# Kernel tuning notes

Hardware: AMD Instinct MI355X
Metric: run time of the kernel (lower is better)

Reference implementation:

```python
import jax, jax.numpy as jnp
import numpy as np

B, S, H = 4, 512, 1024
E, K, I = 8, 2, 2048

def setup_inputs() -> dict:
    key = jax.random.key(0)
    k1, k2, k3, k4, k5 = jax.random.split(key, 5)
    scale_h = 1.0 / np.sqrt(H)
    scale_i = 1.0 / np.sqrt(I)
    return {
        "hidden_states": jax.random.normal(k1, (B, S, H), dtype=jnp.float32),
        "router_w": jax.random.normal(k2, (E, H), dtype=jnp.float32) * scale_h,
        "w_gate": jax.random.normal(k3, (E, H, I), dtype=jnp.float32) * scale_h,
        "w_up": jax.random.normal(k4, (E, H, I), dtype=jnp.float32) * scale_h,
        "w_down": jax.random.normal(k5, (E, I, H), dtype=jnp.float32) * scale_i,
    }

def reference(hidden_states, router_w, w_gate, w_up, w_down):
    b, s, h = hidden_states.shape
    x = hidden_states.reshape(-1, h)              # [T, H] tokens
    T = x.shape[0]

    # ---- RouterTopK: fp32 linear -> softmax over all experts -> top-k ----
    router_logits = x.astype(jnp.float32) @ router_w.T          # [T, E]
    probs = jax.nn.softmax(router_logits, axis=-1)               # [T, E]
    top_vals, top_idx = jax.lax.top_k(probs, K)                  # [T, K]

    # normalize_top_k_affinities (norm_topk_prob=True)
    top_vals = top_vals / jnp.sum(top_vals, axis=-1, keepdims=True)

    # scatter normalized affinities into a dense [T, E] combine matrix
    aff = jnp.zeros((T, E), dtype=x.dtype).at[jnp.arange(T)[:, None], top_idx].set(top_vals.astype(x.dtype))

    # ---- ExpertMLPs: GLU (swiglu) per expert, combine weighted by affinity ----
    # Dense-per-expert computation; non-selected experts contribute 0 via aff.
    gate = jnp.einsum('th,ehi->eti', x, w_gate)                  # [E, T, I]
    up = jnp.einsum('th,ehi->eti', x, w_up)                      # [E, T, I]
    act = jax.nn.silu(gate) * up                                 # [E, T, I]
    expert_out = jnp.einsum('eti,eih->eth', act, w_down)         # [E, T, H]
    out = jnp.einsum('eth,te->th', expert_out, aff)              # [T, H]

    # _reduce_output: all-reduce over TP/world group -> identity single-device
    return out.reshape(b, s, h)
```

## Files before the change

### kernel.cpp

```cpp
#include <hip/hip_runtime.h>
#include <hip/hip_bf16.h>

#define T_TOK 2048
#define H_DIM 1024
#define E_N   8
#define I_DIM 2048
#define GW    4096

#define NT_MAX 24
#define SLOTS  6144

typedef unsigned short u16;
typedef unsigned int   u32;
typedef __bf16 bf16_t;
typedef bf16_t bf16x8 __attribute__((ext_vector_type(8)));
typedef u16    u16x8  __attribute__((ext_vector_type(8)));
typedef u16    u16x4  __attribute__((ext_vector_type(4)));
typedef float  f32x16 __attribute__((ext_vector_type(16)));

#define MFMA32 __builtin_amdgcn_mfma_f32_32x32x16_bf16
#define SB()   __builtin_amdgcn_sched_barrier(0)

__device__ __forceinline__ u16 bfbits(float f) {
    bf16_t b = (bf16_t)f;
    return __builtin_bit_cast(u16, b);
}
__device__ __forceinline__ float bf2f(u16 u) {
    u32 x = ((u32)u) << 16;
    return __builtin_bit_cast(float, x);
}

__device__ __forceinline__ void gload_lds16(const void* g, void* l) {
    __builtin_amdgcn_global_load_lds(
        (const __attribute__((address_space(1))) void*)g,
        (__attribute__((address_space(3))) void*)l, 16, 0, 0);
}

__device__ __forceinline__ int tile_off(int n, int kb) {
    return n * 64 + ((kb ^ ((n >> 1) & 7)) << 3);
}
__device__ __forceinline__ int a_off(int row, int kslot) {
    return row * 64 + ((kslot ^ (row & 7)) << 3);
}

__global__ __launch_bounds__(256) void router_k(
    const float* __restrict__ x, const float* __restrict__ rw,
    int* __restrict__ cnt, int* __restrict__ tok,
    int4* __restrict__ invA, float2* __restrict__ invW,
    u16* __restrict__ xbf)
{
    int wid = threadIdx.x >> 6, lane = threadIdx.x & 63;
    int t = blockIdx.x * 4 + wid;
    const float* xr = x + (size_t)t * H_DIM;
    u16* xbr = xbf + (size_t)t * H_DIM;

    float acc[E_N];
#pragma unroll
    for (int e = 0; e < E_N; e++) acc[e] = 0.f;
#pragma unroll
    for (int j = 0; j < H_DIM / 256; j++) {
        int o = lane * 4 + j * 256;
        float4 xv = *reinterpret_cast<const float4*>(xr + o);
        u16x4 p;
        p[0] = bfbits(xv.x); p[1] = bfbits(xv.y); p[2] = bfbits(xv.z); p[3] = bfbits(xv.w);
        *reinterpret_cast<u16x4*>(xbr + o) = p;
#pragma unroll
        for (int e = 0; e < E_N; e++) {
            float4 wv = *reinterpret_cast<const float4*>(rw + e * H_DIM + o);
            acc[e] += xv.x * wv.x + xv.y * wv.y + xv.z * wv.z + xv.w * wv.w;
        }
    }
#pragma unroll
    for (int e = 0; e < E_N; e++) {
        float v = acc[e];
        for (int off = 32; off; off >>= 1) v += __shfl_xor(v, off);
        acc[e] = v;
    }
    if (lane == 0) {
        int i0 = 0; float m0 = acc[0];
#pragma unroll
        for (int e = 1; e < E_N; e++) if (acc[e] > m0) { m0 = acc[e]; i0 = e; }
        int i1 = -1; float m1 = -INFINITY;
#pragma unroll
        for (int e = 0; e < E_N; e++) if (e != i0 && acc[e] > m1) { m1 = acc[e]; i1 = e; }
        float w0 = 1.f / (1.f + expf(m1 - m0));
        float w1 = 1.f - w0;
        int p0 = atomicAdd(&cnt[i0], 1);
        tok[i0 * T_TOK + p0] = t;
        int p1 = atomicAdd(&cnt[i1], 1);
        tok[i1 * T_TOK + p1] = t;
        invA[t] = make_int4(i0, p0, i1, p1);
        invW[t] = make_float2(w0, w1);
    }
}

__global__ void prefix_k(const int* __restrict__ cnt, int* __restrict__ offs_pad,
                         int* __restrict__ tile_e, int* __restrict__ tile_row0,
                         int* __restrict__ ntiles)
{
    if (threadIdx.x == 0) {
        int s = 0, nt = 0;
        for (int e = 0; e < E_N; e++) {
            offs_pad[e] = s;
            int c = cnt[e];
            int t = (c + 255) >> 8;
            for (int i = 0; i < t; i++) { tile_e[nt] = e; tile_row0[nt] = i * 256; nt++; }
            s += t * 256;
        }
        offs_pad[E_N] = s;
        *ntiles = nt;
    }
}

__global__ __launch_bounds__(512, 4) void gu_k(
    const u16* __restrict__ xbf, const float* __restrict__ wg, const float* __restrict__ wu,
    const int* __restrict__ cnt, const int* __restrict__ offs_pad,
    const int* __restrict__ tile_e, const int* __restrict__ tile_row0,
    const int* __restrict__ ntiles, const int* __restrict__ tok,
    u16* __restrict__ gbuf)
{
    int q = gridDim.x >> 3;
    int phys = blockIdx.x;
    int logical = (phys & 7) * q + (phys >> 3);
    int tb = logical % NT_MAX;
    int p  = logical / NT_MAX;
    if (tb >= *ntiles) return;
    int e = tile_e[tb], row0 = tile_row0[tb];
    int cntE = cnt[e];
    int slot0 = offs_pad[e] + row0;
    int n0 = p * 128;
    int mat  = n0 >> 11;
    int coln = n0 & 2047;

    __shared__ u16 AS[2][16384], BS[8192];

    int tid = threadIdx.x;
    int lane = tid & 63, wid = tid >> 6;
    int wm = wid >> 1, wn = wid & 1;
    int l31 = lane & 31, lh = lane >> 5;

    const u16* asrc[4];
#pragma unroll
    for (int i = 0; i < 4; i++) {
        int row = wid * 32 + i * 8 + (lane >> 3);
        int rc = (row0 + row < cntE) ? (row0 + row) : (cntE - 1);
        asrc[i] = xbf + (size_t)tok[e * T_TOK + rc] * H_DIM
                  + (((lane & 7) ^ ((lane >> 3) & 7)) << 3);
    }
    int s0 = wid * 2048;

    int bn = tid & 127;
    int kq = tid >> 7;
    const float* wsrc = (mat ? wu : wg) + (size_t)e * H_DIM * I_DIM + coln + bn;

    float v[16];

#define BLOAD(t) { \
    _Pragma("unroll") \
    for (int j = 0; j < 16; j++) \
        v[j] = wsrc[(size_t)((t) * 64 + kq * 16 + j) * I_DIM]; }

#define BWRITE() { \
    _Pragma("unroll") \
    for (int jb = 0; jb < 2; jb++) { \
        u16x8 pk; \
        _Pragma("unroll") \
        for (int jj = 0; jj < 8; jj++) pk[jj] = bfbits(v[jb * 8 + jj]); \
        *reinterpret_cast<u16x8*>(&BS[tile_off(bn, kq * 2 + jb)]) = pk; } }

#define ASTAGE(nbuf, t) { \
    _Pragma("unroll") \
    for (int i = 0; i < 4; i++) \
        gload_lds16(asrc[i] + (size_t)(t) * 64, &AS[nbuf][s0 + i * 512]); }

    f32x16 acc[2][2];
#pragma unroll
    for (int a = 0; a < 2; a++)
#pragma unroll
        for (int b = 0; b < 2; b++) acc[a][b] = (f32x16)0.f;

#define CLUSTER(bufi) { \
    _Pragma("unroll") \
    for (int ks = 0; ks < 4; ks++) { \
        bf16x8 af[2], bfr[2]; \
        _Pragma("unroll") \
        for (int mf = 0; mf < 2; mf++) \
            af[mf] = *reinterpret_cast<const bf16x8*>(&AS[bufi][a_off(wm * 64 + mf * 32 + l31, ks * 2 + lh)]); \
        _Pragma("unroll") \
        for (int nf = 0; nf < 2; nf++) \
            bfr[nf] = *reinterpret_cast<const bf16x8*>(&BS[tile_off(wn * 64 + nf * 32 + l31, ks * 2 + lh)]); \
        _Pragma("unroll") \
        for (int mf = 0; mf < 2; mf++) \
            _Pragma("unroll") \
            for (int nf = 0; nf < 2; nf++) \
                acc[mf][nf] = MFMA32(af[mf], bfr[nf], acc[mf][nf], 0, 0, 0); } }

    ASTAGE(0, 0);
    SB();
    BLOAD(0);
    SB();
    BWRITE();
    SB();
    asm volatile("s_waitcnt vmcnt(0) lgkmcnt(0)" ::: "memory");
    __builtin_amdgcn_s_barrier();
    SB();

    for (int t = 0; t < 16; t++) {
        int ab = t & 1;
        bool more = (t + 1) < 16;
        if (more) {
            ASTAGE(ab ^ 1, t + 1);
            SB();
            BLOAD(t + 1);
            SB();
        }
        CLUSTER(ab);
        SB();
        __builtin_amdgcn_s_barrier();
        SB();
        if (more) {
            BWRITE();
            SB();
            asm volatile("s_waitcnt vmcnt(0) lgkmcnt(0)" ::: "memory");
            __builtin_amdgcn_s_barrier();
            SB();
        }
    }
#undef BLOAD
#undef BWRITE
#undef ASTAGE
#undef CLUSTER

#pragma unroll
    for (int mf = 0; mf < 2; mf++)
#pragma unroll
        for (int nf = 0; nf < 2; nf++) {
            int col = n0 + wn * 64 + nf * 32 + l31;
#pragma unroll
            for (int r = 0; r < 16; r++) {
                int rl = wm * 64 + mf * 32 + (r & 3) + 8 * (r >> 2) + 4 * lh;
                gbuf[(size_t)(slot0 + rl) * GW + col] = bfbits(acc[mf][nf][r]);
            }
        }
}

__global__ __launch_bounds__(256) void act_k(u16* __restrict__ gbuf)
{
    int s = blockIdx.x;
    int i = threadIdx.x * 8;
    u16x8 g8 = *reinterpret_cast<const u16x8*>(&gbuf[(size_t)s * GW + i]);
    u16x8 u8 = *reinterpret_cast<const u16x8*>(&gbuf[(size_t)s * GW + 2048 + i]);
    u16x8 o;
#pragma unroll
    for (int j = 0; j < 8; j++) {
        float g = bf2f(g8[j]);
        float u = bf2f(u8[j]);
        o[j] = bfbits(g / (1.f + expf(-g)) * u);
    }
    *reinterpret_cast<u16x8*>(&gbuf[(size_t)s * GW + i]) = o;
}

__global__ __launch_bounds__(512, 4) void down_k(
    const u16* __restrict__ gbuf, const float* __restrict__ wd,
    const int* __restrict__ cnt, const int* __restrict__ offs_pad,
    const int* __restrict__ tile_e, const int* __restrict__ tile_row0,
    const int* __restrict__ ntiles, const int* __restrict__ tok,
    u16* __restrict__ dbuf)
{
    int q = gridDim.x >> 3;
    int phys = blockIdx.x;
    int logical = (phys & 7) * q + (phys >> 3);
    int tb = logical % NT_MAX;
    int rest = logical / NT_MAX;
    int p   = rest & 7;
    int kq4 = rest >> 3;
    if (tb >= *ntiles) return;
    int e = tile_e[tb], row0 = tile_row0[tb];
    int slot0 = offs_pad[e] + row0;
    int h0 = p * 128;

    __shared__ u16 AS[2][16384], BS[8192];

    int tid = threadIdx.x;
    int lane = tid & 63, wid = tid >> 6;
    int wm = wid >> 1, wn = wid & 1;
    int l31 = lane & 31, lh = lane >> 5;

    const u16* asrc[4];
#pragma unroll
    for (int i = 0; i < 4; i++) {
        int row = wid * 32 + i * 8 + (lane >> 3);
        asrc[i] = gbuf + (size_t)(slot0 + row) * GW + kq4 * 512
                  + (((lane & 7) ^ ((lane >> 3) & 7)) << 3);
    }
    int s0 = wid * 2048;

    int bn = tid & 127;
    int kq = tid >> 7;
    const float* dsrc = wd + ((size_t)e * I_DIM + kq4 * 512) * H_DIM + h0 + bn;

    float v[16];

#define BLOAD(t) { \
    _Pragma("unroll") \
    for (int j = 0; j < 16; j++) \
        v[j] = dsrc[(size_t)((t) * 64 + kq * 16 + j) * H_DIM]; }

#define BWRITE() { \
    _Pragma("unroll") \
    for (int jb = 0; jb < 2; jb++) { \
        u16x8 pk; \
        _Pragma("unroll") \
        for (int jj = 0; jj < 8; jj++) pk[jj] = bfbits(v[jb * 8 + jj]); \
        *reinterpret_cast<u16x8*>(&BS[tile_off(bn, kq * 2 + jb)]) = pk; } }

#define ASTAGE(nbuf, t) { \
    _Pragma("unroll") \
    for (int i = 0; i < 4; i++) \
        gload_lds16(asrc[i] + (size_t)(t) * 64, &AS[nbuf][s0 + i * 512]); }

    f32x16 acc[2][2];
#pragma unroll
    for (int a = 0; a < 2; a++)
#pragma unroll
        for (int b = 0; b < 2; b++) acc[a][b] = (f32x16)0.f;

#define CLUSTER(bufi) { \
    _Pragma("unroll") \
    for (int ks = 0; ks < 4; ks++) { \
        bf16x8 af[2], bfr[2]; \
        _Pragma("unroll") \
        for (int mf = 0; mf < 2; mf++) \
            af[mf] = *reinterpret_cast<const bf16x8*>(&AS[bufi][a_off(wm * 64 + mf * 32 + l31, ks * 2 + lh)]); \
        _Pragma("unroll") \
        for (int nf = 0; nf < 2; nf++) \
            bfr[nf] = *reinterpret_cast<const bf16x8*>(&BS[tile_off(wn * 64 + nf * 32 + l31, ks * 2 + lh)]); \
        _Pragma("unroll") \
        for (int mf = 0; mf < 2; mf++) \
            _Pragma("unroll") \
            for (int nf = 0; nf < 2; nf++) \
                acc[mf][nf] = MFMA32(af[mf], bfr[nf], acc[mf][nf], 0, 0, 0); } }

    ASTAGE(0, 0);
    SB();
    BLOAD(0);
    SB();
    BWRITE();
    SB();
    asm volatile("s_waitcnt vmcnt(0) lgkmcnt(0)" ::: "memory");
    __builtin_amdgcn_s_barrier();
    SB();

    for (int t = 0; t < 8; t++) {
        int ab = t & 1;
        bool more = (t + 1) < 8;
        if (more) {
            ASTAGE(ab ^ 1, t + 1);
            SB();
            BLOAD(t + 1);
            SB();
        }
        CLUSTER(ab);
        SB();
        __builtin_amdgcn_s_barrier();
        SB();
        if (more) {
            BWRITE();
            SB();
            asm volatile("s_waitcnt vmcnt(0) lgkmcnt(0)" ::: "memory");
            __builtin_amdgcn_s_barrier();
            SB();
        }
    }
#undef BLOAD
#undef BWRITE
#undef ASTAGE
#undef CLUSTER

#pragma unroll
    for (int mf = 0; mf < 2; mf++)
#pragma unroll
        for (int nf = 0; nf < 2; nf++) {
            int col = h0 + wn * 64 + nf * 32 + l31;
#pragma unroll
            for (int r = 0; r < 16; r++) {
                int rl = wm * 64 + mf * 32 + (r & 3) + 8 * (r >> 2) + 4 * lh;
                dbuf[(size_t)(kq4 * SLOTS + slot0 + rl) * H_DIM + col] = bfbits(acc[mf][nf][r]);
            }
        }
}

__global__ __launch_bounds__(256) void gather_k(
    const u16* __restrict__ dbuf, const int4* __restrict__ invA,
    const float2* __restrict__ invW, const int* __restrict__ offs_pad,
    float* __restrict__ out)
{
    int t = blockIdx.x;
    int h = threadIdx.x * 4;
    int4 ia = invA[t];
    float2 w = invW[t];
    int s0 = offs_pad[ia.x] + ia.y;
    int s1 = offs_pad[ia.z] + ia.w;

    float4 o = make_float4(0.f, 0.f, 0.f, 0.f);
    float* op = &o.x;
#pragma unroll
    for (int qk = 0; qk < 4; qk++) {
        u16x4 a = *reinterpret_cast<const u16x4*>(&dbuf[(size_t)(qk * SLOTS + s0) * H_DIM + h]);
        u16x4 b = *reinterpret_cast<const u16x4*>(&dbuf[(size_t)(qk * SLOTS + s1) * H_DIM + h]);
#pragma unroll
        for (int j = 0; j < 4; j++)
            op[j] += w.x * bf2f(a[j]) + w.y * bf2f(b[j]);
    }
    *reinterpret_cast<float4*>(&out[(size_t)t * H_DIM + h]) = o;
}

extern "C" void kernel_launch(void* const* d_in, const int* in_sizes, int n_in,
                              void* d_out, int out_size, void* d_ws, size_t ws_size,
                              hipStream_t stream)
{
    const float* x  = (const float*)d_in[0];
    const float* rw = (const float*)d_in[1];
    const float* wg = (const float*)d_in[2];
    const float* wu = (const float*)d_in[3];
    const float* wd = (const float*)d_in[4];
    float* out = (float*)d_out;

    char* ws = (char*)d_ws;
    int*    cnt       = (int*)(ws);
    int*    ntiles    = (int*)(ws + 32);
    int*    offs_pad  = (int*)(ws + 64);
    int*    tile_e    = (int*)(ws + 256);
    int*    tile_row0 = (int*)(ws + 512);
    int*    tok       = (int*)(ws + 64 * 1024);
    int4*   invA      = (int4*)(ws + 160 * 1024);
    float2* invW      = (float2*)(ws + 200 * 1024);
    u16*    xbf       = (u16*)(ws + 256 * 1024);
    u16*    gbuf      = (u16*)(ws + 5ull * 1024 * 1024);
    u16*    dbuf      = (u16*)(ws + 53ull * 1024 * 1024);

    size_t need = 102ull * 1024 * 1024;
    if (ws_size < need) return;

    hipMemsetAsync(cnt, 0, 32, stream);

    router_k<<<T_TOK / 4, 256, 0, stream>>>(x, rw, cnt, tok, invA, invW, xbf);
    prefix_k<<<1, 64, 0, stream>>>(cnt, offs_pad, tile_e, tile_row0, ntiles);
    gu_k<<<NT_MAX * (GW / 128), 512, 0, stream>>>(
        xbf, wg, wu, cnt, offs_pad, tile_e, tile_row0, ntiles, tok, gbuf);
    act_k<<<SLOTS, 256, 0, stream>>>(gbuf);
    down_k<<<NT_MAX * (H_DIM / 128) * 4, 512, 0, stream>>>(
        gbuf, wd, cnt, offs_pad, tile_e, tile_row0, ntiles, tok, dbuf);
    gather_k<<<T_TOK, 256, 0, stream>>>(dbuf, invA, invW, offs_pad, out);
}
```

Measured before the change: 211.6 us.

## Restructure expert GEMM main loops into fine-grained software pipeline, halve down split-K

Replaces the per-tile load/compute/store loop in both expert GEMM kernels with an interleaved STEP schedule. Each MFMA sub-step overlaps async A staging, a partial B conversion write into a double-buffered B LDS tile, and register prefetch of B two tiles ahead. MFMAs run under raised priority and waits use a partial vmcnt. The down projection split-K goes from 4 to 2 chunks of 1024, which halves the partial-output buffer and gather reads but doubles per-block work and halves the grid. Launch bounds drop to 2 blocks per SM to fit the extra registers and LDS.

```diff
diff --git a/kernel.cpp b/kernel.cpp
--- a/kernel.cpp
+++ b/kernel.cpp
@@ -112,7 +112,62 @@
     }
 }
 
-__global__ __launch_bounds__(512, 4) void gu_k(
+#define STEP(tt, WSET, LSET, BUFI)                                              \
+  {                                                                             \
+    bool m1 = (tt) + 1 < 16, m2 = (tt) + 2 < 16;                                \
+    _Pragma("unroll")                                                           \
+    for (int p = 0; p < 4; p++) {                                               \
+      bf16x8 af0 = *reinterpret_cast<const bf16x8*>(                            \
+          &AS[BUFI][a_off(wm * 64 + l31, p * 2 + lh)]);                         \
+      bf16x8 af1 = *reinterpret_cast<const bf16x8*>(                            \
+          &AS[BUFI][a_off(wm * 64 + 32 + l31, p * 2 + lh)]);                    \
+      bf16x8 bf0 = *reinterpret_cast<const bf16x8*>(                            \
+          &BS[BUFI][tile_off(wn * 64 + l31, p * 2 + lh)]);                      \
+      bf16x8 bf1 = *reinterpret_cast<const bf16x8*>(                            \
+          &BS[BUFI][tile_off(wn * 64 + 32 + l31, p * 2 + lh)]);                 \
+      SB();                                                                     \
+      if (p == 0 && m1) {                                                       \
+        _Pragma("unroll")                                                       \
+        for (int i = 0; i < 4; i++)                                             \
+          gload_lds16(asrc[i] + (size_t)((tt) + 1) * 64,                        \
+                      &AS[(BUFI) ^ 1][s0 + i * 512]);                           \
+      }                                                                         \
+      SB();                                                                     \
+      if (m1 && (p == 0 || p == 2)) {                                           \
+        u16x8 pk;                                                               \
+        _Pragma("unroll")                                                       \
+        for (int jj = 0; jj < 8; jj++) pk[jj] = bfbits(WSET[(p >> 1) * 8 + jj]);\
+        *reinterpret_cast<u16x8*>(                                              \
+            &BS[(BUFI) ^ 1][tile_off(bn, kq * 2 + (p >> 1))]) = pk;             \
+      }                                                                         \
+      SB();                                                                     \
+      if (m2) {                                                                 \
+        _Pragma("unroll")                                                       \
+        for (int j = 0; j < 4; j++)                                             \
+          LSET[p * 4 + j] =                                                     \
+              bsrc[(size_t)(((tt) + 2) * 64 + kq * 16 + p * 4 + j) * BSTRIDE];  \
+      }                                                                         \
+      SB();                                                                     \
+      __builtin_amdgcn_s_barrier();                                             \
+      asm volatile("s_waitcnt lgkmcnt(0)" ::: "memory");                        \
+      SB();                                                                     \
+      __builtin_amdgcn_s_setprio(1);                                            \
+      acc[0][0] = MFMA32(af0, bf0, acc[0][0], 0, 0, 0);                         \
+      acc[0][1] = MFMA32(af0, bf1, acc[0][1], 0, 0, 0);                         \
+      acc[1][0] = MFMA32(af1, bf0, acc[1][0], 0, 0, 0);                         \
+      acc[1][1] = MFMA32(af1, bf1, acc[1][1], 0, 0, 0);                         \
+      __builtin_amdgcn_s_setprio(0);                                            \
+      SB();                                                                     \
+      if (p == 3) {                                                             \
+        if ((tt) <= 13) { asm volatile("s_waitcnt vmcnt(16)" ::: "memory"); }   \
+        else            { asm volatile("s_waitcnt vmcnt(0)" ::: "memory"); }    \
+      }                                                                         \
+      __builtin_amdgcn_s_barrier();                                             \
+      SB();                                                                     \
+    }                                                                           \
+  }
+
+__global__ __launch_bounds__(512, 2) void gu_k(
     const u16* __restrict__ xbf, const float* __restrict__ wg, const float* __restrict__ wu,
     const int* __restrict__ cnt, const int* __restrict__ offs_pad,
     const int* __restrict__ tile_e, const int* __restrict__ tile_row0,
@@ -132,7 +187,7 @@
     int mat  = n0 >> 11;
     int coln = n0 & 2047;
 
-    __shared__ u16 AS[2][16384], BS[8192];
+    __shared__ u16 AS[2][16384], BS[2][8192];
 
     int tid = threadIdx.x;
     int lane = tid & 63, wid = tid >> 6;
@@ -151,27 +206,10 @@
 
     int bn = tid & 127;
     int kq = tid >> 7;
-    const float* wsrc = (mat ? wu : wg) + (size_t)e * H_DIM * I_DIM + coln + bn;
-
-    float v[16];
-
-#define BLOAD(t) { \
-    _Pragma("unroll") \
-    for (int j = 0; j < 16; j++) \
-        v[j] = wsrc[(size_t)((t) * 64 + kq * 16 + j) * I_DIM]; }
-
-#define BWRITE() { \
-    _Pragma("unroll") \
-    for (int jb = 0; jb < 2; jb++) { \
-        u16x8 pk; \
-        _Pragma("unroll") \
-        for (int jj = 0; jj < 8; jj++) pk[jj] = bfbits(v[jb * 8 + jj]); \
-        *reinterpret_cast<u16x8*>(&BS[tile_off(bn, kq * 2 + jb)]) = pk; } }
-
-#define ASTAGE(nbuf, t) { \
-    _Pragma("unroll") \
-    for (int i = 0; i < 4; i++) \
-        gload_lds16(asrc[i] + (size_t)(t) * 64, &AS[nbuf][s0 + i * 512]); }
+    const float* bsrc = (mat ? wu : wg) + (size_t)e * H_DIM * I_DIM + coln + bn;
+#define BSTRIDE I_DIM
+
+    float v0[16], v1[16];
 
     f32x16 acc[2][2];
 #pragma unroll
@@ -179,57 +217,33 @@
 #pragma unroll
         for (int b = 0; b < 2; b++) acc[a][b] = (f32x16)0.f;
 
-#define CLUSTER(bufi) { \
-    _Pragma("unroll") \
-    for (int ks = 0; ks < 4; ks++) { \
-        bf16x8 af[2], bfr[2]; \
-        _Pragma("unroll") \
-        for (int mf = 0; mf < 2; mf++) \
-            af[mf] = *reinterpret_cast<const bf16x8*>(&AS[bufi][a_off(wm * 64 + mf * 32 + l31, ks * 2 + lh)]); \
-        _Pragma("unroll") \
-        for (int nf = 0; nf < 2; nf++) \
-            bfr[nf] = *reinterpret_cast<const bf16x8*>(&BS[tile_off(wn * 64 + nf * 32 + l31, ks * 2 + lh)]); \
-        _Pragma("unroll") \
-        for (int mf = 0; mf < 2; mf++) \
-            _Pragma("unroll") \
-            for (int nf = 0; nf < 2; nf++) \
-                acc[mf][nf] = MFMA32(af[mf], bfr[nf], acc[mf][nf], 0, 0, 0); } }
-
-    ASTAGE(0, 0);
-    SB();
-    BLOAD(0);
-    SB();
-    BWRITE();
+#pragma unroll
+    for (int i = 0; i < 4; i++)
+        gload_lds16(asrc[i], &AS[0][s0 + i * 512]);
+    SB();
+#pragma unroll
+    for (int j = 0; j < 16; j++) v0[j] = bsrc[(size_t)(kq * 16 + j) * BSTRIDE];
+    SB();
+#pragma unroll
+    for (int j = 0; j < 16; j++) v1[j] = bsrc[(size_t)(64 + kq * 16 + j) * BSTRIDE];
+    SB();
+#pragma unroll
+    for (int jb = 0; jb < 2; jb++) {
+        u16x8 pk;
+#pragma unroll
+        for (int jj = 0; jj < 8; jj++) pk[jj] = bfbits(v0[jb * 8 + jj]);
+        *reinterpret_cast<u16x8*>(&BS[0][tile_off(bn, kq * 2 + jb)]) = pk;
+    }
     SB();
     asm volatile("s_waitcnt vmcnt(0) lgkmcnt(0)" ::: "memory");
     __builtin_amdgcn_s_barrier();
     SB();
 
-    for (int t = 0; t < 16; t++) {
-        int ab = t & 1;
-        bool more = (t + 1) < 16;
-        if (more) {
-            ASTAGE(ab ^ 1, t + 1);
-            SB();
-            BLOAD(t + 1);
-            SB();
-        }
-        CLUSTER(ab);
-        SB();
-        __builtin_amdgcn_s_barrier();
-        SB();
-        if (more) {
-            BWRITE();
-            SB();
-            asm volatile("s_waitcnt vmcnt(0) lgkmcnt(0)" ::: "memory");
-            __builtin_amdgcn_s_barrier();
-            SB();
-        }
-    }
-#undef BLOAD
-#undef BWRITE
-#undef ASTAGE
-#undef CLUSTER
+    for (int t2 = 0; t2 < 16; t2 += 2) {
+        STEP(t2,     v1, v0, 0);
+        STEP(t2 + 1, v0, v1, 1);
+    }
+#undef BSTRIDE
 
 #pragma unroll
     for (int mf = 0; mf < 2; mf++)
@@ -260,7 +274,7 @@
     *reinterpret_cast<u16x8*>(&gbuf[(size_t)s * GW + i]) = o;
 }
 
-__global__ __launch_bounds__(512, 4) void down_k(
+__global__ __launch_bounds__(512, 2) void down_k(
     const u16* __restrict__ gbuf, const float* __restrict__ wd,
     const int* __restrict__ cnt, const int* __restrict__ offs_pad,
     const int* __restrict__ tile_e, const int* __restrict__ tile_row0,
@@ -272,14 +286,14 @@
     int logical = (phys & 7) * q + (phys >> 3);
     int tb = logical % NT_MAX;
     int rest = logical / NT_MAX;
-    int p   = rest & 7;
-    int kq4 = rest >> 3;
+    int p  = rest & 7;
+    int kh = rest >> 3;
     if (tb >= *ntiles) return;
     int e = tile_e[tb], row0 = tile_row0[tb];
     int slot0 = offs_pad[e] + row0;
     int h0 = p * 128;
 
-    __shared__ u16 AS[2][16384], BS[8192];
+    __shared__ u16 AS[2][16384], BS[2][8192];
 
     int tid = threadIdx.x;
     int lane = tid & 63, wid = tid >> 6;
@@ -290,34 +304,17 @@
 #pragma unroll
     for (int i = 0; i < 4; i++) {
         int row = wid * 32 + i * 8 + (lane >> 3);
-        asrc[i] = gbuf + (size_t)(slot0 + row) * GW + kq4 * 512
+        asrc[i] = gbuf + (size_t)(slot0 + row) * GW + kh * 1024
                   + (((lane & 7) ^ ((lane >> 3) & 7)) << 3);
     }
     int s0 = wid * 2048;
 
     int bn = tid & 127;
     int kq = tid >> 7;
-    const float* dsrc = wd + ((size_t)e * I_DIM + kq4 * 512) * H_DIM + h0 + bn;
-
-    float v[16];
-
-#define BLOAD(t) { \
-    _Pragma("unroll") \
-    for (int j = 0; j < 16; j++) \
-        v[j] = dsrc[(size_t)((t) * 64 + kq * 16 + j) * H_DIM]; }
-
-#define BWRITE() { \
-    _Pragma("unroll") \
-    for (int jb = 0; jb < 2; jb++) { \
-        u16x8 pk; \
-        _Pragma("unroll") \
-        for (int jj = 0; jj < 8; jj++) pk[jj] = bfbits(v[jb * 8 + jj]); \
-        *reinterpret_cast<u16x8*>(&BS[tile_off(bn, kq * 2 + jb)]) = pk; } }
-
-#define ASTAGE(nbuf, t) { \
-    _Pragma("unroll") \
-    for (int i = 0; i < 4; i++) \
-        gload_lds16(asrc[i] + (size_t)(t) * 64, &AS[nbuf][s0 + i * 512]); }
+    const float* bsrc = wd + ((size_t)e * I_DIM + kh * 1024) * H_DIM + h0 + bn;
+#define BSTRIDE H_DIM
+
+    float v0[16], v1[16];
 
     f32x16 acc[2][2];
 #pragma unroll
@@ -325,57 +322,33 @@
 #pragma unroll
         for (int b = 0; b < 2; b++) acc[a][b] = (f32x16)0.f;
 
-#define CLUSTER(bufi) { \
-    _Pragma("unroll") \
-    for (int ks = 0; ks < 4; ks++) { \
-        bf16x8 af[2], bfr[2]; \
-        _Pragma("unroll") \
-        for (int mf = 0; mf < 2; mf++) \
-            af[mf] = *reinterpret_cast<const bf16x8*>(&AS[bufi][a_off(wm * 64 + mf * 32 + l31, ks * 2 + lh)]); \
-        _Pragma("unroll") \
-        for (int nf = 0; nf < 2; nf++) \
-            bfr[nf] = *reinterpret_cast<const bf16x8*>(&BS[tile_off(wn * 64 + nf * 32 + l31, ks * 2 + lh)]); \
-        _Pragma("unroll") \
-        for (int mf = 0; mf < 2; mf++) \
-            _Pragma("unroll") \
-            for (int nf = 0; nf < 2; nf++) \
-                acc[mf][nf] = MFMA32(af[mf], bfr[nf], acc[mf][nf], 0, 0, 0); } }
-
-    ASTAGE(0, 0);
-    SB();
-    BLOAD(0);
-    SB();
-    BWRITE();
+#pragma unroll
+    for (int i = 0; i < 4; i++)
+        gload_lds16(asrc[i], &AS[0][s0 + i * 512]);
+    SB();
+#pragma unroll
+    for (int j = 0; j < 16; j++) v0[j] = bsrc[(size_t)(kq * 16 + j) * BSTRIDE];
+    SB();
+#pragma unroll
+    for (int j = 0; j < 16; j++) v1[j] = bsrc[(size_t)(64 + kq * 16 + j) * BSTRIDE];
+    SB();
+#pragma unroll
+    for (int jb = 0; jb < 2; jb++) {
+        u16x8 pk;
+#pragma unroll
+        for (int jj = 0; jj < 8; jj++) pk[jj] = bfbits(v0[jb * 8 + jj]);
+        *reinterpret_cast<u16x8*>(&BS[0][tile_off(bn, kq * 2 + jb)]) = pk;
+    }
     SB();
     asm volatile("s_waitcnt vmcnt(0) lgkmcnt(0)" ::: "memory");
     __builtin_amdgcn_s_barrier();
     SB();
 
-    for (int t = 0; t < 8; t++) {
-        int ab = t & 1;
-        bool more = (t + 1) < 8;
-        if (more) {
-            ASTAGE(ab ^ 1, t + 1);
-            SB();
-            BLOAD(t + 1);
-            SB();
-        }
-        CLUSTER(ab);
-        SB();
-        __builtin_amdgcn_s_barrier();
-        SB();
-        if (more) {
-            BWRITE();
-            SB();
-            asm volatile("s_waitcnt vmcnt(0) lgkmcnt(0)" ::: "memory");
-            __builtin_amdgcn_s_barrier();
-            SB();
-        }
-    }
-#undef BLOAD
-#undef BWRITE
-#undef ASTAGE
-#undef CLUSTER
+    for (int t2 = 0; t2 < 16; t2 += 2) {
+        STEP(t2,     v1, v0, 0);
+        STEP(t2 + 1, v0, v1, 1);
+    }
+#undef BSTRIDE
 
 #pragma unroll
     for (int mf = 0; mf < 2; mf++)
@@ -385,7 +358,7 @@
 #pragma unroll
             for (int r = 0; r < 16; r++) {
                 int rl = wm * 64 + mf * 32 + (r & 3) + 8 * (r >> 2) + 4 * lh;
-                dbuf[(size_t)(kq4 * SLOTS + slot0 + rl) * H_DIM + col] = bfbits(acc[mf][nf][r]);
+                dbuf[(size_t)(kh * SLOTS + slot0 + rl) * H_DIM + col] = bfbits(acc[mf][nf][r]);
             }
         }
 }
@@ -402,16 +375,16 @@
     int s0 = offs_pad[ia.x] + ia.y;
     int s1 = offs_pad[ia.z] + ia.w;
 
-    float4 o = make_float4(0.f, 0.f, 0.f, 0.f);
+    u16x4 a0 = *reinterpret_cast<const u16x4*>(&dbuf[(size_t)s0 * H_DIM + h]);
+    u16x4 a1 = *reinterpret_cast<const u16x4*>(&dbuf[(size_t)(SLOTS + s0) * H_DIM + h]);
+    u16x4 b0 = *reinterpret_cast<const u16x4*>(&dbuf[(size_t)s1 * H_DIM + h]);
+    u16x4 b1 = *reinterpret_cast<const u16x4*>(&dbuf[(size_t)(SLOTS + s1) * H_DIM + h]);
+
+    float4 o;
     float* op = &o.x;
 #pragma unroll
-    for (int qk = 0; qk < 4; qk++) {
-        u16x4 a = *reinterpret_cast<const u16x4*>(&dbuf[(size_t)(qk * SLOTS + s0) * H_DIM + h]);
-        u16x4 b = *reinterpret_cast<const u16x4*>(&dbuf[(size_t)(qk * SLOTS + s1) * H_DIM + h]);
-#pragma unroll
-        for (int j = 0; j < 4; j++)
-            op[j] += w.x * bf2f(a[j]) + w.y * bf2f(b[j]);
-    }
+    for (int j = 0; j < 4; j++)
+        op[j] = w.x * (bf2f(a0[j]) + bf2f(a1[j])) + w.y * (bf2f(b0[j]) + bf2f(b1[j]));
     *reinterpret_cast<float4*>(&out[(size_t)t * H_DIM + h]) = o;
 }
 
@@ -439,7 +412,7 @@
     u16*    gbuf      = (u16*)(ws + 5ull * 1024 * 1024);
     u16*    dbuf      = (u16*)(ws + 53ull * 1024 * 1024);
 
-    size_t need = 102ull * 1024 * 1024;
+    size_t need = 78ull * 1024 * 1024;
     if (ws_size < need) return;
 
     hipMemsetAsync(cnt, 0, 32, stream);
@@ -449,7 +422,7 @@
     gu_k<<<NT_MAX * (GW / 128), 512, 0, stream>>>(
         xbf, wg, wu, cnt, offs_pad, tile_e, tile_row0, ntiles, tok, gbuf);
     act_k<<<SLOTS, 256, 0, stream>>>(gbuf);
-    down_k<<<NT_MAX * (H_DIM / 128) * 4, 512, 0, stream>>>(
+    down_k<<<NT_MAX * (H_DIM / 128) * 2, 512, 0, stream>>>(
         gbuf, wd, cnt, offs_pad, tile_e, tile_row0, ntiles, tok, dbuf);
     gather_k<<<T_TOK, 256, 0, stream>>>(dbuf, invA, invW, offs_pad, out);
 }
```

After: 254.7 us. +20.4%, slower.
